# Performance work log

Hardware: AMD Instinct MI355X
Metric: run time of the kernel (lower is better)

The kernel has to match this reference:

```python
import jax, jax.numpy as jnp
import numpy as np

QMAX = 127.0

def _sym_quantize(t):
    # per-tensor symmetric int8 fake-quant: returns (quantized values as float, scale)
    scale = jnp.max(jnp.abs(t)) / QMAX
    q = jnp.clip(jnp.round(t / scale), -QMAX, QMAX)
    return q, scale

def setup_inputs() -> dict:
    key = jax.random.key(0)
    k1, k2, k3 = jax.random.split(key, 3)
    TOKENS, IN_F, OUT_F = 4096, 4096, 4096
    x = jax.random.normal(k1, (TOKENS, IN_F), dtype=jnp.float32)
    # int8-valued weight buffer (stored int32 for portability), symmetric range
    quantized_weight = jax.random.randint(k2, (OUT_F, IN_F), -127, 128, dtype=jnp.int32)
    weight_scale = jnp.float32(0.01)  # scalar per-tensor weight scale buffer
    bias = jax.random.normal(k3, (OUT_F,), dtype=jnp.float32)
    return {"x": x, "quantized_weight": quantized_weight,
            "weight_scale": weight_scale, "bias": bias}

def reference(x, quantized_weight, weight_scale, bias):
    q_x, x_scale = _sym_quantize(x)                      # [T, In] fake-quant activations
    w = quantized_weight.astype(jnp.float32)             # [Out, In]
    out = jnp.matmul(q_x, w.T)                           # fp32 GEMM on int8-valued operands
    out = out * (x_scale * weight_scale)                 # dequant scaling
    out = out + bias
    return out
```

## Files before the change

### kernel.cpp

```cpp
#include <hip/hip_runtime.h>

typedef __attribute__((ext_vector_type(4))) int int4v;

#define NB_MAX 1024

__device__ __forceinline__ void async_ld16(const void* g, void* l) {
  __builtin_amdgcn_global_load_lds(
      (const __attribute__((address_space(1))) void*)g,
      (__attribute__((address_space(3))) void*)l,
      16, 0, 0);
}

__global__ void absmax_partial_kernel(const float* __restrict__ x,
                                      float* __restrict__ partial, int n4) {
  const float4* x4 = (const float4*)x;
  float m = 0.0f;
  for (int i = blockIdx.x * blockDim.x + threadIdx.x; i < n4;
       i += gridDim.x * blockDim.x) {
    float4 v = x4[i];
    m = fmaxf(m, fabsf(v.x));
    m = fmaxf(m, fabsf(v.y));
    m = fmaxf(m, fabsf(v.z));
    m = fmaxf(m, fabsf(v.w));
  }
#pragma unroll
  for (int off = 32; off > 0; off >>= 1)
    m = fmaxf(m, __shfl_down(m, off, 64));
  __shared__ float wmax[4];
  const int wid = threadIdx.x >> 6;
  if ((threadIdx.x & 63) == 0) wmax[wid] = m;
  __syncthreads();
  if (threadIdx.x == 0)
    partial[blockIdx.x] =
        fmaxf(fmaxf(wmax[0], wmax[1]), fmaxf(wmax[2], wmax[3]));
}

__device__ __forceinline__ float reduce_partials(const float* partial) {
  __shared__ float smax;
  float m = 0.0f;
  for (int i = threadIdx.x; i < NB_MAX; i += blockDim.x)
    m = fmaxf(m, partial[i]);
#pragma unroll
  for (int off = 32; off > 0; off >>= 1)
    m = fmaxf(m, __shfl_down(m, off, 64));
  __shared__ float wmax[4];
  const int wid = threadIdx.x >> 6;
  if ((threadIdx.x & 63) == 0) wmax[wid] = m;
  __syncthreads();
  if (threadIdx.x == 0)
    smax = fmaxf(fmaxf(wmax[0], wmax[1]), fmaxf(wmax[2], wmax[3]));
  __syncthreads();
  return smax;
}

__global__ void quant_pack_kernel(const float* __restrict__ x,
                                  const int* __restrict__ w,
                                  const float* __restrict__ partial,
                                  float* __restrict__ scale_slot,
                                  int* __restrict__ qx, int* __restrict__ qw,
                                  int nx4, int nw4) {
  const float scale = reduce_partials(partial) / 127.0f;
  const int i = blockIdx.x * blockDim.x + threadIdx.x;
  if (i == 0) *scale_slot = scale;
  if (i < nx4) {
    float4 v = ((const float4*)x)[i];
    int q0 = (int)fminf(fmaxf(rintf(v.x / scale), -127.0f), 127.0f);
    int q1 = (int)fminf(fmaxf(rintf(v.y / scale), -127.0f), 127.0f);
    int q2 = (int)fminf(fmaxf(rintf(v.z / scale), -127.0f), 127.0f);
    int q3 = (int)fminf(fmaxf(rintf(v.w / scale), -127.0f), 127.0f);
    unsigned int p = (unsigned int)(q0 & 255) |
                     ((unsigned int)(q1 & 255) << 8) |
                     ((unsigned int)(q2 & 255) << 16) |
                     ((unsigned int)(q3 & 255) << 24);
    qx[i] = (int)p;
  }
  if (i < nw4) {
    int4 v = ((const int4*)w)[i];
    unsigned int p = (unsigned int)(v.x & 255) |
                     ((unsigned int)(v.y & 255) << 8) |
                     ((unsigned int)(v.z & 255) << 16) |
                     ((unsigned int)(v.w & 255) << 24);
    qw[i] = (int)p;
  }
}

__global__ __launch_bounds__(256) void gemm_i8_kernel(
    const signed char* __restrict__ A,
    const signed char* __restrict__ B,
    const float* __restrict__ bias,
    const float* __restrict__ scale_slot,
    const float* __restrict__ wscale,
    float* __restrict__ out, int K, int N) {
  __shared__ signed char As[128 * 64];
  __shared__ signed char Bs[128 * 64];

  const int tid = threadIdx.x;
  const int lane = tid & 63;
  const int wid = tid >> 6;
  const int row0 = blockIdx.y * 128;
  const int col0 = blockIdx.x * 128;
  const int wm = (wid >> 1) * 64;
  const int wn = (wid & 1) * 64;

  int4v acc[4][4] = {};

  signed char* lA = As + wid * 2048;
  signed char* lB = Bs + wid * 2048;
  const int kb_s = ((lane & 3) ^ ((lane >> 3) & 3)) * 16;
  const signed char* gA =
      A + (long)(row0 + wid * 32 + (lane >> 2)) * K + kb_s;
  const signed char* gB =
      B + (long)(col0 + wid * 32 + (lane >> 2)) * K + kb_s;

  const int swz_f = (lane >> 1) & 3;
  const int fa = (wm + (lane & 15)) * 64 + (((lane >> 4) ^ swz_f) << 4);
  const int fb = (wn + (lane & 15)) * 64 + (((lane >> 4) ^ swz_f) << 4);

  for (int k0 = 0; k0 < K; k0 += 64) {
    __syncthreads();
    async_ld16(gA, lA);
    async_ld16(gA + 16 * (long)K, lA + 1024);
    async_ld16(gB, lB);
    async_ld16(gB + 16 * (long)K, lB + 1024);
    gA += 64;
    gB += 64;
    asm volatile("s_waitcnt vmcnt(0)" ::: "memory");
    __syncthreads();

    int4v a[4], b[4];
#pragma unroll
    for (int i = 0; i < 4; i++) {
      a[i] = *(const int4v*)(As + fa + i * 16 * 64);
      b[i] = *(const int4v*)(Bs + fb + i * 16 * 64);
    }
#pragma unroll
    for (int i = 0; i < 4; i++)
#pragma unroll
      for (int j = 0; j < 4; j++)
        acc[i][j] =
            __builtin_amdgcn_mfma_i32_16x16x64_i8(a[i], b[j], acc[i][j], 0, 0, 0);
  }

  const float s = scale_slot[0] * wscale[0];
  const int orow = row0 + wm + ((lane >> 4) << 2);
  const int ocol0 = col0 + wn + (lane & 15);
#pragma unroll
  for (int j = 0; j < 4; j++) {
    const int c = ocol0 + j * 16;
    const float bv = bias[c];
#pragma unroll
    for (int i = 0; i < 4; i++) {
#pragma unroll
      for (int r = 0; r < 4; r++) {
        out[(long)(orow + i * 16 + r) * N + c] = (float)acc[i][j][r] * s + bv;
      }
    }
  }
}

extern "C" void kernel_launch(void* const* d_in, const int* in_sizes, int n_in,
                              void* d_out, int out_size, void* d_ws,
                              size_t ws_size, hipStream_t stream) {
  const float* x = (const float*)d_in[0];
  const int* w = (const int*)d_in[1];
  const float* wscale = (const float*)d_in[2];
  const float* bias = (const float*)d_in[3];
  float* out = (float*)d_out;

  const int OUT_F = in_sizes[3];
  const int IN_F = in_sizes[1] / OUT_F;
  const int TOKENS = in_sizes[0] / IN_F;

  float* partial = (float*)d_ws;
  float* scale_slot = partial + NB_MAX;
  signed char* qx = (signed char*)d_ws + 8192;
  signed char* qw = qx + (size_t)TOKENS * IN_F;

  const int nx4 = TOKENS * IN_F / 4;
  const int nw4 = OUT_F * IN_F / 4;

  absmax_partial_kernel<<<NB_MAX, 256, 0, stream>>>(x, partial, nx4);

  const int nmax = nx4 > nw4 ? nx4 : nw4;
  quant_pack_kernel<<<(nmax + 255) / 256, 256, 0, stream>>>(
      x, w, partial, scale_slot, (int*)qx, (int*)qw, nx4, nw4);

  dim3 grid(OUT_F / 128, TOKENS / 128);
  gemm_i8_kernel<<<grid, 256, 0, stream>>>(qx, qw, bias, scale_slot, wscale,
                                           out, IN_F, OUT_F);
}
```

Before: 284.8 us.

## Double-buffer LDS tiles to overlap global loads with MFMA compute

Doubles the shared-memory A/B tiles and restructures the K loop into a two-stage ping-pong: the next K tile is issued as async global-to-LDS loads while MFMAs run on the current buffer. The explicit vmcnt(0) wait is removed, so the code now relies on the barrier to make the async LDS writes visible before they are read. The final iteration wraps its prefetch offset to zero, which adds one redundant tile load. LDS use per block doubles, which may limit how many blocks fit on a CU.

```diff
diff --git a/kernel.cpp b/kernel.cpp
--- a/kernel.cpp
+++ b/kernel.cpp
@@ -91,8 +91,8 @@
     const float* __restrict__ scale_slot,
     const float* __restrict__ wscale,
     float* __restrict__ out, int K, int N) {
-  __shared__ signed char As[128 * 64];
-  __shared__ signed char Bs[128 * 64];
+  __shared__ signed char As[2][128 * 64];
+  __shared__ signed char Bs[2][128 * 64];
 
   const int tid = threadIdx.x;
   const int lane = tid & 63;
@@ -104,42 +104,57 @@
 
   int4v acc[4][4] = {};
 
-  signed char* lA = As + wid * 2048;
-  signed char* lB = Bs + wid * 2048;
   const int kb_s = ((lane & 3) ^ ((lane >> 3) & 3)) * 16;
-  const signed char* gA =
+  const signed char* gA0 =
       A + (long)(row0 + wid * 32 + (lane >> 2)) * K + kb_s;
-  const signed char* gB =
+  const signed char* gA1 = gA0 + 16 * (long)K;
+  const signed char* gB0 =
       B + (long)(col0 + wid * 32 + (lane >> 2)) * K + kb_s;
+  const signed char* gB1 = gB0 + 16 * (long)K;
+  const int ldsw = wid * 2048;
 
   const int swz_f = (lane >> 1) & 3;
   const int fa = (wm + (lane & 15)) * 64 + (((lane >> 4) ^ swz_f) << 4);
   const int fb = (wn + (lane & 15)) * 64 + (((lane >> 4) ^ swz_f) << 4);
 
-  for (int k0 = 0; k0 < K; k0 += 64) {
+  async_ld16(gA0, &As[0][ldsw]);
+  async_ld16(gA1, &As[0][ldsw + 1024]);
+  async_ld16(gB0, &Bs[0][ldsw]);
+  async_ld16(gB1, &Bs[0][ldsw + 1024]);
+  int koff = 64;
+
+#define PREFETCH(buf)                                   \
+  {                                                     \
+    const int ko = (koff < K) ? koff : 0;               \
+    async_ld16(gA0 + ko, &As[buf][ldsw]);               \
+    async_ld16(gA1 + ko, &As[buf][ldsw + 1024]);        \
+    async_ld16(gB0 + ko, &Bs[buf][ldsw]);               \
+    async_ld16(gB1 + ko, &Bs[buf][ldsw + 1024]);        \
+    koff += 64;                                         \
+  }
+
+#define STEP(buf)                                               \
+  {                                                             \
+    int4v a[4], b[4];                                           \
+    _Pragma("unroll") for (int i = 0; i < 4; i++) {             \
+      a[i] = *(const int4v*)(&As[buf][fa + i * 16 * 64]);       \
+      b[i] = *(const int4v*)(&Bs[buf][fb + i * 16 * 64]);       \
+    }                                                           \
+    _Pragma("unroll") for (int i = 0; i < 4; i++)               \
+        _Pragma("unroll") for (int j = 0; j < 4; j++) acc[i][j] = \
+        __builtin_amdgcn_mfma_i32_16x16x64_i8(a[i], b[j], acc[i][j], 0, 0, 0); \
+  }
+
+  for (int k0 = 0; k0 < K; k0 += 128) {
     __syncthreads();
-    async_ld16(gA, lA);
-    async_ld16(gA + 16 * (long)K, lA + 1024);
-    async_ld16(gB, lB);
-    async_ld16(gB + 16 * (long)K, lB + 1024);
-    gA += 64;
-    gB += 64;
-    asm volatile("s_waitcnt vmcnt(0)" ::: "memory");
+    PREFETCH(1)
+    STEP(0)
     __syncthreads();
-
-    int4v a[4], b[4];
-#pragma unroll
-    for (int i = 0; i < 4; i++) {
-      a[i] = *(const int4v*)(As + fa + i * 16 * 64);
-      b[i] = *(const int4v*)(Bs + fb + i * 16 * 64);
-    }
-#pragma unroll
-    for (int i = 0; i < 4; i++)
-#pragma unroll
-      for (int j = 0; j < 4; j++)
-        acc[i][j] =
-            __builtin_amdgcn_mfma_i32_16x16x64_i8(a[i], b[j], acc[i][j], 0, 0, 0);
-  }
+    PREFETCH(0)
+    STEP(1)
+  }
+#undef PREFETCH
+#undef STEP
 
   const float s = scale_slot[0] * wscale[0];
   const int orow = row0 + wm + ((lane >> 4) << 2);
```

Measured after the change: 281.1 us. Within noise of the previous version (-1.3%).
